# Kernel tuning notes

Hardware: AMD Instinct MI355X
Metric: run time of the kernel (lower is better)

## Reference

```python
import jax, jax.numpy as jnp
import numpy as np

B, N, P, E = 64, 512, 256, 4096          # batch, nodes (stations), partition nodes, edges
NUM_NWP, LP, F = 8, 16, 32               # num_nwp, local_points, local_cnn_dims
NT, ED, H, W = 8, 8, 64, 8               # num_temp, edge_feature_dims, decf_mlp_hidden, weight_function_dim
G, RH = 64, 256                          # gnn_dim, readout_hid_dim
H1, Q = 128, 9                           # mlp_hid_dim1, num quantiles


def setup_inputs() -> dict:
    key = jax.random.key(0)
    ks = iter(jax.random.split(key, 40))
    def rn(shape, s=0.05):
        return jax.random.normal(next(ks), shape, dtype=jnp.float32) * s
    # one-hot incidence matrices: each edge has one left (partition) node and one right node
    lidx = jax.random.randint(next(ks), (E,), 0, P)
    ridx = jax.random.randint(next(ks), (E,), 0, N)
    linc = jnp.zeros((P, E), jnp.float32).at[lidx, jnp.arange(E)].set(1.0)
    rinc = jnp.zeros((E, N), jnp.float32).at[jnp.arange(E), ridx].set(1.0)
    inp = {
        "x1": jax.random.normal(next(ks), (B, NUM_NWP * N, LP), dtype=jnp.float32),
        "x2": jax.random.normal(next(ks), (B, NT), dtype=jnp.float32),
        # LocalConv1D grouped conv (torch OIW layout: [Cout, Cin/groups, K])
        "conv_w": rn((F * N, NUM_NWP, LP)), "conv_b": rn((F * N,)),
        # WDSGCN2 edge-weight MLP
        "k1_w": rn((H, ED)), "k1_b": rn((H,)),
        "k2_w": rn((H, NT)),
        "k3_w": rn((H, F)),
        "k4_w": rn((H, F)),
        "k5_w": rn((W, H)), "k5_b": rn((W,)),
        "gc_w": rn((G, F * W)), "gc_b": rn((G,)),
        # readout
        "r0_w": rn((RH, G * P)),
        "r1_w": rn((RH, NT)), "r1_b": rn((RH,)),
        "r2_w": rn((RH, P)),
        "r3_w": rn((P, RH)), "r3_b": rn((P,)),
        # SMlp (forward uses l1 -> ELU -> l3 only)
        "l1_w": rn((H1, NT + G)), "l1_b": rn((H1,)),
        "l3_w": rn((Q, H1)), "l3_b": rn((Q,)),
        # buffers
        "ef": jax.random.normal(next(ks), (E, ED + 1), dtype=jnp.float32),
        "linc": linc,
        "rinc": rinc,
        "cap_feature": jax.random.normal(next(ks), (P,), dtype=jnp.float32),
        "partition_idx": jnp.arange(P, dtype=jnp.int32) * (N // P),
    }
    return inp


def reference(x1, x2, conv_w, conv_b, k1_w, k1_b, k2_w, k3_w, k4_w, k5_w, k5_b,
              gc_w, gc_b, r0_w, r1_w, r1_b, r2_w, r3_w, r3_b,
              l1_w, l1_b, l3_w, l3_b, ef, linc, rinc, cap_feature, partition_idx):
    b = x1.shape[0]
    # --- LocalConv1D: grouped conv1d (valid padding, output length 1) + ReLU ---
    y = jax.lax.conv_general_dilated(x1, conv_w, (1,), 'VALID',
                                     dimension_numbers=('NCH', 'OIH', 'NCH'),
                                     feature_group_count=N)
    x = jax.nn.relu(y + conv_b[None, :, None]).reshape(b, N, F)      # [B,N,F]
    # --- WDSGCN2: per-edge weight kernel ---
    kern = ef[:, :-1] @ k1_w.T + k1_b                                # [E,H]
    kern = kern[None] + (x2 @ k2_w.T)[:, None, :]                    # [B,E,H]
    xp = x[:, partition_idx, :]                                      # [B,P,F]
    kern = kern + jnp.einsum('pe,bpf->bef', linc, xp) @ k3_w.T       # left-node feats
    rx = jnp.einsum('en,bnf->bef', rinc, x)                          # right-node feats [B,E,F]
    kern = kern + rx @ k4_w.T
    kern = jax.nn.relu(jax.nn.leaky_relu(kern, 0.02) @ k5_w.T + k5_b)  # [B,E,W]
    # --- message = kernel (outer) right-node features, aggregated by left incidence ---
    msg = kern[:, :, :, None] * rx[:, :, None, :]                    # [B,E,W,F]
    agg = jnp.einsum('pe,bewf->bpwf', linc, msg).reshape(b, P, W * F)
    yg = jax.nn.relu(agg @ gc_w.T + gc_b)                            # [B,P,G]
    # --- readout attention over partition nodes ---
    h = yg.reshape(b, -1) @ r0_w.T + (x2 @ r1_w.T + r1_b) + cap_feature @ r2_w.T
    wt = jax.nn.relu(jax.nn.leaky_relu(h, 0.01) @ r3_w.T + r3_b)     # [B,P]
    res = jnp.einsum('bp,bpg->bg', wt, yg)                           # [B,G]
    # --- SMlp head ---
    z = jnp.concatenate([res, x2], axis=1)
    z = jax.nn.elu(z @ l1_w.T + l1_b)
    return z @ l3_w.T + l3_b                                         # [B,Q]
```

## Files before the change

kernel.cpp:

```cpp
#include <hip/hip_runtime.h>
#include <math.h>

#define B_ 64
#define N_ 512
#define P_ 256
#define E_ 4096
#define F_ 32
#define H_ 64
#define W_ 8
#define G_ 64
#define RH_ 256

#define X_OFF   0
#define T4_OFF  (X_OFF + N_*B_*F_)
#define T3_OFF  (T4_OFF + N_*B_*H_)
#define KB_OFF  (T3_OFF + P_*B_*H_)
#define KW_OFF  (KB_OFF + E_*H_)
#define YG_OFF  (KW_OFF + E_*B_*W_)
#define HB_OFF  (YG_OFF + B_*P_*G_)
#define RES_OFF (HB_OFF + B_*RH_)
#define INT_OFF (RES_OFF + 4*B_*G_)
#define PART_OFF (INT_OFF + 20480)

__global__ __launch_bounds__(256) void k_dc(const float* __restrict__ linc,
    const float* __restrict__ rinc, int* __restrict__ lidx, int* __restrict__ ridx,
    const float* __restrict__ x1, const float* __restrict__ conv_w,
    const float* __restrict__ conv_b, float* __restrict__ x) {
  __shared__ float wsm[32 * 132];
  __shared__ float xsm[8192];
  int blk = blockIdx.x, t = threadIdx.x;
  if (blk < 3072) {
    int i4 = blk * 256 + t;
    const int L4 = (P_ * E_) / 4;
    if (i4 < L4) {
      float4 v = ((const float4*)linc)[i4];
      int i = i4 * 4;
      int p = i >> 12, e = i & 4095;
      if (v.x != 0.0f) lidx[e]     = p;
      if (v.y != 0.0f) lidx[e + 1] = p;
      if (v.z != 0.0f) lidx[e + 2] = p;
      if (v.w != 0.0f) lidx[e + 3] = p;
    } else {
      int j4 = i4 - L4;
      float4 v = ((const float4*)rinc)[j4];
      int j = j4 * 4;
      int e = j >> 9, n = j & 511;
      if (v.x != 0.0f) ridx[e] = n;
      if (v.y != 0.0f) ridx[e] = n + 1;
      if (v.z != 0.0f) ridx[e] = n + 2;
      if (v.w != 0.0f) ridx[e] = n + 3;
    }
    return;
  }
  int n = blk - 3072;
  for (int i = t; i < 1024; i += 256) {
    int f = i >> 5, j = i & 31;
    ((float4*)wsm)[f * 33 + j] = ((const float4*)(conv_w + n * 4096))[i];
  }
  for (int i = t; i < 2048; i += 256) {
    int b = i >> 5, j = i & 31;
    ((float4*)xsm)[i] = ((const float4*)(x1 + b * 65536 + n * 128))[j];
  }
  __syncthreads();
  int f = t & 31, bq = t >> 5;
  float cb = conv_b[n * 32 + f];
  float acc[8];
#pragma unroll
  for (int bi = 0; bi < 8; bi++) acc[bi] = cb;
  const float4* wf4 = (const float4*)wsm + f * 33;
  const float4* xb4 = (const float4*)xsm + bq * 256;
#pragma unroll 4
  for (int k4 = 0; k4 < 32; k4++) {
    float4 wv = wf4[k4];
#pragma unroll
    for (int bi = 0; bi < 8; bi++) {
      float4 xv = xb4[bi * 32 + k4];
      acc[bi] += wv.x * xv.x + wv.y * xv.y + wv.z * xv.z + wv.w * xv.w;
    }
  }
#pragma unroll
  for (int bi = 0; bi < 8; bi++) {
    int b = bq * 8 + bi;
    x[n * 2048 + b * 32 + f] = fmaxf(acc[bi], 0.0f);
  }
}

__global__ __launch_bounds__(1024) void k_lists(const int* __restrict__ lidx,
    const int* __restrict__ ridx, int* __restrict__ part_start,
    int* __restrict__ part_edges, int* __restrict__ r_s) {
  __shared__ int cnt[256];
  __shared__ int buf[256];
  __shared__ int cur[256];
  int t = threadIdx.x;
  if (t < 256) cnt[t] = 0;
  __syncthreads();
  for (int e = t; e < E_; e += 1024) atomicAdd(&cnt[lidx[e]], 1);
  __syncthreads();
  if (t < 256) buf[t] = cnt[t];
  __syncthreads();
  for (int off = 1; off < 256; off <<= 1) {
    int add = 0;
    if (t < 256 && t >= off) add = buf[t - off];
    __syncthreads();
    if (t < 256) buf[t] += add;
    __syncthreads();
  }
  if (t < 256) {
    part_start[t + 1] = buf[t];
    if (t == 0) part_start[0] = 0;
    cur[t] = buf[t] - cnt[t];
  }
  __syncthreads();
  for (int e = t; e < E_; e += 1024) {
    int p = lidx[e];
    int pos = atomicAdd(&cur[p], 1);
    part_edges[pos] = e;
  }
  __syncthreads();
  for (int pos = t; pos < E_; pos += 1024) r_s[pos] = ridx[part_edges[pos]];
}

__global__ __launch_bounds__(256) void k_prep(
    const float* __restrict__ x, const int* __restrict__ pidx,
    const float* __restrict__ k3_w, const float* __restrict__ k4_w,
    const float* __restrict__ x2, const float* __restrict__ k2_w,
    const float* __restrict__ ef, const float* __restrict__ k1_w,
    const float* __restrict__ k1_b,
    const float* __restrict__ r1_w, const float* __restrict__ r1_b,
    const float* __restrict__ r2_w, const float* __restrict__ cap,
    float* __restrict__ t4, float* __restrict__ t3, float* __restrict__ kb,
    float* __restrict__ hbuf) {
  __shared__ float xsh[2048];
  __shared__ float wsh[64 * 36];
  __shared__ float x2s[512];
  __shared__ float k2s[512];
  int blk = blockIdx.x, t = threadIdx.x;
  if (blk < 768) {
    bool isT4 = blk < 512;
    int n = isT4 ? blk : pidx[blk - 512];
    const float* wmat = isT4 ? k4_w : k3_w;
    float* outp = isT4 ? (t4 + blk * 4096) : (t3 + (blk - 512) * 4096);
    for (int i = t; i < 512; i += 256) {
      ((float4*)xsh)[i] = ((const float4*)(x + n * 2048))[i];
      int h = i >> 3, j = i & 7;
      ((float4*)wsh)[h * 9 + j] = ((const float4*)wmat)[i];
    }
    if (isT4) {
      for (int i = t; i < 128; i += 256) {
        ((float4*)x2s)[i] = ((const float4*)x2)[i];
        ((float4*)k2s)[i] = ((const float4*)k2_w)[i];
      }
    }
    __syncthreads();
    int h = t & 63, bq = t >> 6;
    float wreg[32];
#pragma unroll
    for (int j = 0; j < 8; j++) {
      float4 v = ((float4*)wsh)[h * 9 + j];
      wreg[4 * j] = v.x; wreg[4 * j + 1] = v.y; wreg[4 * j + 2] = v.z; wreg[4 * j + 3] = v.w;
    }
    float w2[8];
    if (isT4) {
      float4 u = ((float4*)k2s)[h * 2], v = ((float4*)k2s)[h * 2 + 1];
      w2[0] = u.x; w2[1] = u.y; w2[2] = u.z; w2[3] = u.w;
      w2[4] = v.x; w2[5] = v.y; w2[6] = v.z; w2[7] = v.w;
    }
    for (int bi = 0; bi < 16; bi++) {
      int b = bq * 16 + bi;
      float acc = 0.0f;
#pragma unroll
      for (int j = 0; j < 8; j++) {
        float4 xv = ((float4*)xsh)[b * 8 + j];
        acc += xv.x * wreg[4 * j] + xv.y * wreg[4 * j + 1] +
               xv.z * wreg[4 * j + 2] + xv.w * wreg[4 * j + 3];
      }
      if (isT4) {
        float4 u = ((float4*)x2s)[b * 2], v = ((float4*)x2s)[b * 2 + 1];
        acc += u.x * w2[0] + u.y * w2[1] + u.z * w2[2] + u.w * w2[3] +
               v.x * w2[4] + v.y * w2[5] + v.z * w2[6] + v.w * w2[7];
      }
      outp[b * 64 + h] = acc;
    }
  } else if (blk < 1792) {
    int o = (blk - 768) * 256 + t;
    int e = o >> 6, h = o & 63;
    float acc = k1_b[h];
    const float* er = ef + e * 9;
    const float* kr = k1_w + h * 8;
#pragma unroll
    for (int d = 0; d < 8; d++) acc += er[d] * kr[d];
    kb[o] = acc;
  } else {
    int o = (blk - 1792) * 256 + t;
    int rh = o & 255;
    float acc = r1_b[rh];
    const float* xr = x2 + (o >> 8) * 8;
    const float* rr = r1_w + rh * 8;
#pragma unroll
    for (int d = 0; d < 8; d++) acc += xr[d] * rr[d];
    const float* r2r = r2_w + rh * 256;
    for (int p4 = 0; p4 < 64; p4++) {
      float4 cv = ((const float4*)cap)[p4];
      float4 rv = ((const float4*)r2r)[p4];
      acc += cv.x * rv.x + cv.y * rv.y + cv.z * rv.z + cv.w * rv.w;
    }
    hbuf[o] = acc;
  }
}

__global__ __launch_bounds__(256) void k_edge(
    const float* __restrict__ kb, const float* __restrict__ t3,
    const float* __restrict__ t4, const float* __restrict__ k5_w,
    const float* __restrict__ k5_b, const int* __restrict__ lidx,
    const int* __restrict__ ridx, const int* __restrict__ part_edges,
    float* __restrict__ kw_s) {
  __shared__ float k5t[4 * 520];
  int pos0 = blockIdx.x * 4, t = threadIdx.x;
  for (int i = t; i < 512; i += 256) {
    int h = i >> 3, w = i & 7;
    float v = k5_w[w * 64 + h];
#pragma unroll
    for (int qq = 0; qq < 4; qq++) k5t[qq * 520 + i] = v;
  }
  int q = t & 3, b = t >> 2;
  const float* kq = k5t + q * 520 + q * 128;
  float kb5_0 = k5_b[2 * q], kb5_1 = k5_b[2 * q + 1];
  __syncthreads();
  for (int ei = 0; ei < 4; ei++) {
    int pos = pos0 + ei;
    int e = part_edges[pos];
    int p = lidx[e], r = ridx[e];
    const float4* kb4 = (const float4*)(kb + e * 64 + q * 16);
    const float4* t34 = (const float4*)(t3 + p * 4096 + b * 64 + q * 16);
    const float4* t44 = (const float4*)(t4 + r * 4096 + b * 64 + q * 16);
    float lk[16];
#pragma unroll
    for (int j4 = 0; j4 < 4; j4++) {
      float4 a = kb4[j4], c = t34[j4], d = t44[j4];
      float v;
      v = a.x + c.x + d.x; lk[j4 * 4 + 0] = v > 0.0f ? v : 0.02f * v;
      v = a.y + c.y + d.y; lk[j4 * 4 + 1] = v > 0.0f ? v : 0.02f * v;
      v = a.z + c.z + d.z; lk[j4 * 4 + 2] = v > 0.0f ? v : 0.02f * v;
      v = a.w + c.w + d.w; lk[j4 * 4 + 3] = v > 0.0f ? v : 0.02f * v;
    }
    float pw[8] = {0, 0, 0, 0, 0, 0, 0, 0};
#pragma unroll
    for (int j = 0; j < 16; j++) {
      float4 u = *(const float4*)(kq + j * 8);
      float4 v = *(const float4*)(kq + j * 8 + 4);
      float l = lk[j];
      pw[0] += l * u.x; pw[1] += l * u.y; pw[2] += l * u.z; pw[3] += l * u.w;
      pw[4] += l * v.x; pw[5] += l * v.y; pw[6] += l * v.z; pw[7] += l * v.w;
    }
#pragma unroll
    for (int w = 0; w < 8; w++) {
      pw[w] += __shfl_xor(pw[w], 1);
      pw[w] += __shfl_xor(pw[w], 2);
    }
    float2 o;
    o.x = fmaxf(pw[2 * q] + kb5_0, 0.0f);
    o.y = fmaxf(pw[2 * q + 1] + kb5_1, 0.0f);
    *(float2*)(kw_s + pos * 512 + t * 2) = o;
  }
}

__global__ __launch_bounds__(256) void k_agg(
    const float* __restrict__ x, const float* __restrict__ kw_s,
    const int* __restrict__ r_s, const int* __restrict__ part_start,
    const float* __restrict__ gc_w, const float* __restrict__ gc_b,
    float* __restrict__ yg) {
  __shared__ float accS[32 * 256];
  int blk = blockIdx.x, t = threadIdx.x;
  int p = blk & 255, bsub = blk >> 8;
  int bl = t >> 3, s = t & 7;
  int b = bsub * 32 + bl;
  float acc[32];
#pragma unroll
  for (int j = 0; j < 32; j++) acc[j] = 0.0f;
  int s0 = part_start[p], s1 = part_start[p + 1];
  int r = (s0 < s1) ? r_s[s0] : 0;
  for (int pos = s0; pos < s1; pos++) {
    int r_n = (pos + 1 < s1) ? r_s[pos + 1] : 0;
    float kv = kw_s[pos * 512 + b * 8 + s];
    const float4* xp = (const float4*)(x + r * 2048 + b * 32);
    float4 x0 = xp[0], x1 = xp[1], x2 = xp[2], x3 = xp[3];
    float4 x4 = xp[4], x5 = xp[5], x6 = xp[6], x7 = xp[7];
    float xa[32];
    xa[0] = x0.x; xa[1] = x0.y; xa[2] = x0.z; xa[3] = x0.w;
    xa[4] = x1.x; xa[5] = x1.y; xa[6] = x1.z; xa[7] = x1.w;
    xa[8] = x2.x; xa[9] = x2.y; xa[10] = x2.z; xa[11] = x2.w;
    xa[12] = x3.x; xa[13] = x3.y; xa[14] = x3.z; xa[15] = x3.w;
    xa[16] = x4.x; xa[17] = x4.y; xa[18] = x4.z; xa[19] = x4.w;
    xa[20] = x5.x; xa[21] = x5.y; xa[22] = x5.z; xa[23] = x5.w;
    xa[24] = x6.x; xa[25] = x6.y; xa[26] = x6.z; xa[27] = x6.w;
    xa[28] = x7.x; xa[29] = x7.y; xa[30] = x7.z; xa[31] = x7.w;
#pragma unroll
    for (int j = 0; j < 32; j++) acc[j] += kv * xa[j];
    r = r_n;
  }
  int swz = bl >> 2;
#pragma unroll
  for (int j = 0; j < 4; j++) {
    int oct = s * 4 + j;
    int os = oct ^ swz;
    float* dst = accS + bl * 256 + os * 8;
    *(float4*)dst = make_float4(acc[j * 8], acc[j * 8 + 1], acc[j * 8 + 2], acc[j * 8 + 3]);
    *(float4*)(dst + 4) = make_float4(acc[j * 8 + 4], acc[j * 8 + 5], acc[j * 8 + 6], acc[j * 8 + 7]);
  }
  __syncthreads();
  int lane = t & 63, wv = t >> 6;
  int bg = lane >> 3, gg = lane & 7;
  int g0 = wv * 16 + gg * 2;
  const float* gw0 = gc_w + g0 * 256;
  const float* gw1 = gw0 + 256;
  float ac[4][2];
#pragma unroll
  for (int i = 0; i < 4; i++) { ac[i][0] = 0.0f; ac[i][1] = 0.0f; }
  for (int oct = 0; oct < 32; oct++) {
    float av[4][8];
#pragma unroll
    for (int i = 0; i < 4; i++) {
      int bli = bg * 4 + i;
      int os = oct ^ bg;
      const float* srcp = accS + bli * 256 + os * 8;
      float4 va = *(const float4*)srcp;
      float4 vb = *(const float4*)(srcp + 4);
      av[i][0] = va.x; av[i][1] = va.y; av[i][2] = va.z; av[i][3] = va.w;
      av[i][4] = vb.x; av[i][5] = vb.y; av[i][6] = vb.z; av[i][7] = vb.w;
    }
    float4 b0a = *(const float4*)(gw0 + oct * 8);
    float4 b0b = *(const float4*)(gw0 + oct * 8 + 4);
    float4 b1a = *(const float4*)(gw1 + oct * 8);
    float4 b1b = *(const float4*)(gw1 + oct * 8 + 4);
    float bv0[8] = {b0a.x, b0a.y, b0a.z, b0a.w, b0b.x, b0b.y, b0b.z, b0b.w};
    float bv1[8] = {b1a.x, b1a.y, b1a.z, b1a.w, b1b.x, b1b.y, b1b.z, b1b.w};
#pragma unroll
    for (int kk = 0; kk < 8; kk++) {
#pragma unroll
      for (int i = 0; i < 4; i++) {
        float a = av[i][kk];
        ac[i][0] += a * bv0[kk];
        ac[i][1] += a * bv1[kk];
      }
    }
  }
  float gb0 = gc_b[g0], gb1 = gc_b[g0 + 1];
#pragma unroll
  for (int i = 0; i < 4; i++) {
    int bb = bsub * 32 + bg * 4 + i;
    float2 o;
    o.x = fmaxf(ac[i][0] + gb0, 0.0f);
    o.y = fmaxf(ac[i][1] + gb1, 0.0f);
    *(float2*)(yg + bb * 16384 + p * 64 + g0) = o;
  }
}

__global__ __launch_bounds__(256) void k_r0(const float* __restrict__ yg,
    const float* __restrict__ r0_w, float* __restrict__ part) {
  __shared__ float ygs[32 * 69];
  __shared__ float wts[32 * 260];
  int kc = blockIdx.x, t = threadIdx.x;
  int k0 = kc * 32;
  {
    int c = t >> 5, rr = t & 31;
    for (int rd = 0; rd < 8; rd++) {
      int rh = rd * 32 + rr;
      float4 v = *(const float4*)(r0_w + rh * 16384 + k0 + c * 4);
      wts[(4 * c + 0) * 260 + rh] = v.x;
      wts[(4 * c + 1) * 260 + rh] = v.y;
      wts[(4 * c + 2) * 260 + rh] = v.z;
      wts[(4 * c + 3) * 260 + rh] = v.w;
    }
  }
  {
    int b = t >> 2, kq = t & 3;
    const float* src = yg + b * 16384 + k0 + kq * 8;
#pragma unroll
    for (int uu = 0; uu < 2; uu++) {
      float4 v = *(const float4*)(src + uu * 4);
      int kk = kq * 8 + uu * 4;
      ygs[(kk + 0) * 69 + b] = v.x;
      ygs[(kk + 1) * 69 + b] = v.y;
      ygs[(kk + 2) * 69 + b] = v.z;
      ygs[(kk + 3) * 69 + b] = v.w;
    }
  }
  __syncthreads();
  int lane = t & 63, wv = t >> 6;
  int b8 = lane & 7, r8 = lane >> 3;
  const float* yp = ygs + b8 * 8;
  const float* wp = wts + wv * 64 + r8 * 8;
  float acc[8][8];
#pragma unroll
  for (int i = 0; i < 8; i++)
#pragma unroll
    for (int j = 0; j < 8; j++) acc[i][j] = 0.0f;
#pragma unroll 2
  for (int k = 0; k < 32; k++) {
    float4 ya = *(const float4*)(yp + k * 69);
    float4 yb = *(const float4*)(yp + k * 69 + 4);
    float4 wa = *(const float4*)(wp + k * 260);
    float4 wb = *(const float4*)(wp + k * 260 + 4);
    float yv[8] = {ya.x, ya.y, ya.z, ya.w, yb.x, yb.y, yb.z, yb.w};
    float wr[8] = {wa.x, wa.y, wa.z, wa.w, wb.x, wb.y, wb.z, wb.w};
#pragma unroll
    for (int i = 0; i < 8; i++)
#pragma unroll
      for (int j = 0; j < 8; j++) acc[i][j] += yv[i] * wr[j];
  }
  float* pb = part + kc * 16384 + wv * 64 + r8 * 8;
#pragma unroll
  for (int i = 0; i < 8; i++) {
    float4 s0 = make_float4(acc[i][0], acc[i][1], acc[i][2], acc[i][3]);
    float4 s1 = make_float4(acc[i][4], acc[i][5], acc[i][6], acc[i][7]);
    float* pp = pb + (b8 * 8 + i) * 256;
    *(float4*)pp = s0;
    *(float4*)(pp + 4) = s1;
  }
}

__global__ __launch_bounds__(256) void k_r0red(const float* __restrict__ part,
    float* __restrict__ hbuf) {
  int blk = blockIdx.x;
  int oq = blk & 63, kq = blk >> 6;
  int o = oq * 256 + threadIdx.x;
  float s = 0.0f;
  const float* pp = part + kq * 64 * 16384 + o;
#pragma unroll 8
  for (int kc = 0; kc < 64; kc++) s += pp[kc * 16384];
  atomicAdd(&hbuf[o], s);
}

__global__ __launch_bounds__(256) void k_wt_res(const float* __restrict__ hbuf,
    const float* __restrict__ r3_w, const float* __restrict__ r3_b,
    const float* __restrict__ yg, float* __restrict__ res4) {
  __shared__ float hs[256];
  __shared__ float wts[64];
  __shared__ float red[256];
  int blk = blockIdx.x;
  int bb = blk >> 2, pq = blk & 3;
  int t = threadIdx.x;
  float hv = hbuf[bb * 256 + t];
  hs[t] = hv > 0.0f ? hv : 0.01f * hv;
  __syncthreads();
  int pl = t >> 2, c = t & 3;
  int pp = pq * 64 + pl;
  const float4* wrow = (const float4*)(r3_w + pp * 256 + c * 64);
  const float4* h4 = (const float4*)(hs) + c * 16;
  float a = 0.0f;
#pragma unroll
  for (int j = 0; j < 16; j++) {
    float4 w4 = wrow[j], hh = h4[j];
    a += hh.x * w4.x + hh.y * w4.y + hh.z * w4.z + hh.w * w4.w;
  }
  a += __shfl_xor(a, 1);
  a += __shfl_xor(a, 2);
  if (c == 0) wts[pl] = fmaxf(a + r3_b[pp], 0.0f);
  __syncthreads();
  int g = t & 63, ch = t >> 6;
  float r = 0.0f;
  const float* ygp = yg + bb * 16384 + pq * 4096 + g;
#pragma unroll
  for (int pi = 0; pi < 16; pi++) {
    int pl2 = ch * 16 + pi;
    r += wts[pl2] * ygp[pl2 * 64];
  }
  red[t] = r;
  __syncthreads();
  if (t < 64)
    res4[pq * 4096 + bb * 64 + t] = red[t] + red[t + 64] + red[t + 128] + red[t + 192];
}

__global__ __launch_bounds__(128) void k_final(const float* __restrict__ res4,
    const float* __restrict__ x2, const float* __restrict__ l1_w,
    const float* __restrict__ l1_b, const float* __restrict__ l3_w,
    const float* __restrict__ l3_b, float* __restrict__ out) {
  __shared__ float zs[128];
  int bb = blockIdx.x, t = threadIdx.x;
  float acc = l1_b[t];
  const float* wrow = l1_w + t * 72;
  const float* rr = res4 + bb * 64;
#pragma unroll 8
  for (int j = 0; j < 64; j++) {
    float rv = rr[j] + rr[4096 + j] + rr[8192 + j] + rr[12288 + j];
    acc += rv * wrow[j];
  }
  const float* xr = x2 + bb * 8;
#pragma unroll
  for (int j = 0; j < 8; j++) acc += xr[j] * wrow[64 + j];
  zs[t] = acc > 0.0f ? acc : expm1f(acc);
  __syncthreads();
  if (t < 9) {
    float o = l3_b[t];
    const float* w3 = l3_w + t * 128;
    for (int j = 0; j < 128; j++) o += zs[j] * w3[j];
    out[bb * 9 + t] = o;
  }
}

extern "C" void kernel_launch(void* const* d_in, const int* in_sizes, int n_in,
                              void* d_out, int out_size, void* d_ws, size_t ws_size,
                              hipStream_t stream) {
  (void)in_sizes; (void)n_in; (void)out_size; (void)ws_size;
  const float* x1     = (const float*)d_in[0];
  const float* x2     = (const float*)d_in[1];
  const float* conv_w = (const float*)d_in[2];
  const float* conv_b = (const float*)d_in[3];
  const float* k1_w   = (const float*)d_in[4];
  const float* k1_b   = (const float*)d_in[5];
  const float* k2_w   = (const float*)d_in[6];
  const float* k3_w   = (const float*)d_in[7];
  const float* k4_w   = (const float*)d_in[8];
  const float* k5_w   = (const float*)d_in[9];
  const float* k5_b   = (const float*)d_in[10];
  const float* gc_w   = (const float*)d_in[11];
  const float* gc_b   = (const float*)d_in[12];
  const float* r0_w   = (const float*)d_in[13];
  const float* r1_w   = (const float*)d_in[14];
  const float* r1_b   = (const float*)d_in[15];
  const float* r2_w   = (const float*)d_in[16];
  const float* r3_w   = (const float*)d_in[17];
  const float* r3_b   = (const float*)d_in[18];
  const float* l1_w   = (const float*)d_in[19];
  const float* l1_b   = (const float*)d_in[20];
  const float* l3_w   = (const float*)d_in[21];
  const float* l3_b   = (const float*)d_in[22];
  const float* ef     = (const float*)d_in[23];
  const float* linc   = (const float*)d_in[24];
  const float* rinc   = (const float*)d_in[25];
  const float* cap    = (const float*)d_in[26];
  const int*   pidx   = (const int*)d_in[27];
  float* out = (float*)d_out;

  float* ws   = (float*)d_ws;
  float* xbuf = ws + X_OFF;
  float* t4   = ws + T4_OFF;
  float* t3   = ws + T3_OFF;
  float* kb   = ws + KB_OFF;
  float* kw_s = ws + KW_OFF;
  float* yg   = ws + YG_OFF;
  float* hbuf = ws + HB_OFF;
  float* res4 = ws + RES_OFF;
  float* part = ws + PART_OFF;
  int* ib = (int*)(ws + INT_OFF);
  int* lidx = ib;
  int* ridx = ib + 4096;
  int* part_start = ib + 8192;
  int* part_edges = ib + 8704;
  int* r_s = ib + 12800;

  hipLaunchKernelGGL(k_dc, dim3(3584), dim3(256), 0, stream,
                     linc, rinc, lidx, ridx, x1, conv_w, conv_b, xbuf);
  hipLaunchKernelGGL(k_lists, dim3(1), dim3(1024), 0, stream,
                     lidx, ridx, part_start, part_edges, r_s);
  hipLaunchKernelGGL(k_prep, dim3(1856), dim3(256), 0, stream,
                     xbuf, pidx, k3_w, k4_w, x2, k2_w, ef, k1_w, k1_b,
                     r1_w, r1_b, r2_w, cap, t4, t3, kb, hbuf);
  hipLaunchKernelGGL(k_edge, dim3(1024), dim3(256), 0, stream,
                     kb, t3, t4, k5_w, k5_b, lidx, ridx, part_edges, kw_s);
  hipLaunchKernelGGL(k_agg, dim3(512), dim3(256), 0, stream,
                     xbuf, kw_s, r_s, part_start, gc_w, gc_b, yg);
  hipLaunchKernelGGL(k_r0, dim3(512), dim3(256), 0, stream, yg, r0_w, part);
  hipLaunchKernelGGL(k_r0red, dim3(512), dim3(256), 0, stream, part, hbuf);
  hipLaunchKernelGGL(k_wt_res, dim3(256), dim3(256), 0, stream, hbuf, r3_w, r3_b, yg, res4);
  hipLaunchKernelGGL(k_final, dim3(64), dim3(128), 0, stream,
                     res4, x2, l1_w, l1_b, l3_w, l3_b, out);
}
```

Measured before the change: 286.5 us.

## Split k_agg work across more blocks and unroll edge loop by four

The aggregation kernel now handles 16 batch rows per block instead of 32, with each thread covering half the feature dimension. This doubles the grid to 1024 blocks and halves the per-thread accumulator registers. The edge loop is unrolled by four so index and weight loads are batched ahead of the gathers, giving more memory-level parallelism. The cost is that gc_w is re-read by twice as many blocks, and each thread issues more separate gather loads.

```diff
diff --git a/kernel.cpp b/kernel.cpp
--- a/kernel.cpp
+++ b/kernel.cpp
@@ -269,90 +269,91 @@
     const int* __restrict__ r_s, const int* __restrict__ part_start,
     const float* __restrict__ gc_w, const float* __restrict__ gc_b,
     float* __restrict__ yg) {
-  __shared__ float accS[32 * 256];
+  __shared__ float accS[16 * 256];
   int blk = blockIdx.x, t = threadIdx.x;
   int p = blk & 255, bsub = blk >> 8;
-  int bl = t >> 3, s = t & 7;
-  int b = bsub * 32 + bl;
-  float acc[32];
-#pragma unroll
-  for (int j = 0; j < 32; j++) acc[j] = 0.0f;
+  int bl = t >> 4, s = t & 15;
+  int b = bsub * 16 + bl;
+  int w = s >> 1, fh = s & 1;
+  float acc[16];
+#pragma unroll
+  for (int j = 0; j < 16; j++) acc[j] = 0.0f;
   int s0 = part_start[p], s1 = part_start[p + 1];
-  int r = (s0 < s1) ? r_s[s0] : 0;
-  for (int pos = s0; pos < s1; pos++) {
-    int r_n = (pos + 1 < s1) ? r_s[pos + 1] : 0;
-    float kv = kw_s[pos * 512 + b * 8 + s];
-    const float4* xp = (const float4*)(x + r * 2048 + b * 32);
+  const float* xb = x + b * 32 + fh * 16;
+  const float* kwp = kw_s + b * 8 + w;
+  int pos = s0;
+  for (; pos + 3 < s1; pos += 4) {
+    int rr[4];
+    float kvv[4];
+    rr[0] = r_s[pos];     rr[1] = r_s[pos + 1];
+    rr[2] = r_s[pos + 2]; rr[3] = r_s[pos + 3];
+    kvv[0] = kwp[(pos) * 512];     kvv[1] = kwp[(pos + 1) * 512];
+    kvv[2] = kwp[(pos + 2) * 512]; kvv[3] = kwp[(pos + 3) * 512];
+#pragma unroll
+    for (int i = 0; i < 4; i++) {
+      const float4* xp = (const float4*)(xb + rr[i] * 2048);
+      float4 x0 = xp[0], x1 = xp[1], x2 = xp[2], x3 = xp[3];
+      float kv = kvv[i];
+      acc[0]  += kv * x0.x; acc[1]  += kv * x0.y; acc[2]  += kv * x0.z; acc[3]  += kv * x0.w;
+      acc[4]  += kv * x1.x; acc[5]  += kv * x1.y; acc[6]  += kv * x1.z; acc[7]  += kv * x1.w;
+      acc[8]  += kv * x2.x; acc[9]  += kv * x2.y; acc[10] += kv * x2.z; acc[11] += kv * x2.w;
+      acc[12] += kv * x3.x; acc[13] += kv * x3.y; acc[14] += kv * x3.z; acc[15] += kv * x3.w;
+    }
+  }
+  for (; pos < s1; pos++) {
+    int r = r_s[pos];
+    float kv = kwp[pos * 512];
+    const float4* xp = (const float4*)(xb + r * 2048);
     float4 x0 = xp[0], x1 = xp[1], x2 = xp[2], x3 = xp[3];
-    float4 x4 = xp[4], x5 = xp[5], x6 = xp[6], x7 = xp[7];
-    float xa[32];
-    xa[0] = x0.x; xa[1] = x0.y; xa[2] = x0.z; xa[3] = x0.w;
-    xa[4] = x1.x; xa[5] = x1.y; xa[6] = x1.z; xa[7] = x1.w;
-    xa[8] = x2.x; xa[9] = x2.y; xa[10] = x2.z; xa[11] = x2.w;
-    xa[12] = x3.x; xa[13] = x3.y; xa[14] = x3.z; xa[15] = x3.w;
-    xa[16] = x4.x; xa[17] = x4.y; xa[18] = x4.z; xa[19] = x4.w;
-    xa[20] = x5.x; xa[21] = x5.y; xa[22] = x5.z; xa[23] = x5.w;
-    xa[24] = x6.x; xa[25] = x6.y; xa[26] = x6.z; xa[27] = x6.w;
-    xa[28] = x7.x; xa[29] = x7.y; xa[30] = x7.z; xa[31] = x7.w;
-#pragma unroll
-    for (int j = 0; j < 32; j++) acc[j] += kv * xa[j];
-    r = r_n;
-  }
-  int swz = bl >> 2;
-#pragma unroll
-  for (int j = 0; j < 4; j++) {
-    int oct = s * 4 + j;
+    acc[0]  += kv * x0.x; acc[1]  += kv * x0.y; acc[2]  += kv * x0.z; acc[3]  += kv * x0.w;
+    acc[4]  += kv * x1.x; acc[5]  += kv * x1.y; acc[6]  += kv * x1.z; acc[7]  += kv * x1.w;
+    acc[8]  += kv * x2.x; acc[9]  += kv * x2.y; acc[10] += kv * x2.z; acc[11] += kv * x2.w;
+    acc[12] += kv * x3.x; acc[13] += kv * x3.y; acc[14] += kv * x3.z; acc[15] += kv * x3.w;
+  }
+  int swz = (bl >> 1) & 3;
+#pragma unroll
+  for (int j = 0; j < 2; j++) {
+    int oct = s * 2 + j;
     int os = oct ^ swz;
     float* dst = accS + bl * 256 + os * 8;
     *(float4*)dst = make_float4(acc[j * 8], acc[j * 8 + 1], acc[j * 8 + 2], acc[j * 8 + 3]);
-    *(float4*)(dst + 4) = make_float4(acc[j * 8 + 4], acc[j * 8 + 5], acc[j * 8 + 6], acc[j * 8 + 7]);
+    *(float4*)(dst + 4) =
+        make_float4(acc[j * 8 + 4], acc[j * 8 + 5], acc[j * 8 + 6], acc[j * 8 + 7]);
   }
   __syncthreads();
   int lane = t & 63, wv = t >> 6;
-  int bg = lane >> 3, gg = lane & 7;
+  int q = lane >> 3, gg = lane & 7;
   int g0 = wv * 16 + gg * 2;
   const float* gw0 = gc_w + g0 * 256;
   const float* gw1 = gw0 + 256;
-  float ac[4][2];
-#pragma unroll
-  for (int i = 0; i < 4; i++) { ac[i][0] = 0.0f; ac[i][1] = 0.0f; }
+  float ac00 = 0.0f, ac01 = 0.0f, ac10 = 0.0f, ac11 = 0.0f;
+  int row0 = q * 2, row1 = q * 2 + 1;
+  int sz = q & 3;
   for (int oct = 0; oct < 32; oct++) {
-    float av[4][8];
-#pragma unroll
-    for (int i = 0; i < 4; i++) {
-      int bli = bg * 4 + i;
-      int os = oct ^ bg;
-      const float* srcp = accS + bli * 256 + os * 8;
-      float4 va = *(const float4*)srcp;
-      float4 vb = *(const float4*)(srcp + 4);
-      av[i][0] = va.x; av[i][1] = va.y; av[i][2] = va.z; av[i][3] = va.w;
-      av[i][4] = vb.x; av[i][5] = vb.y; av[i][6] = vb.z; av[i][7] = vb.w;
-    }
-    float4 b0a = *(const float4*)(gw0 + oct * 8);
-    float4 b0b = *(const float4*)(gw0 + oct * 8 + 4);
-    float4 b1a = *(const float4*)(gw1 + oct * 8);
-    float4 b1b = *(const float4*)(gw1 + oct * 8 + 4);
+    int os = oct ^ sz;
+    const float* s0p = accS + row0 * 256 + os * 8;
+    const float* s1p = accS + row1 * 256 + os * 8;
+    float4 a0a = *(const float4*)s0p, a0b = *(const float4*)(s0p + 4);
+    float4 a1a = *(const float4*)s1p, a1b = *(const float4*)(s1p + 4);
+    float4 b0a = *(const float4*)(gw0 + oct * 8), b0b = *(const float4*)(gw0 + oct * 8 + 4);
+    float4 b1a = *(const float4*)(gw1 + oct * 8), b1b = *(const float4*)(gw1 + oct * 8 + 4);
+    float av0[8] = {a0a.x, a0a.y, a0a.z, a0a.w, a0b.x, a0b.y, a0b.z, a0b.w};
+    float av1[8] = {a1a.x, a1a.y, a1a.z, a1a.w, a1b.x, a1b.y, a1b.z, a1b.w};
     float bv0[8] = {b0a.x, b0a.y, b0a.z, b0a.w, b0b.x, b0b.y, b0b.z, b0b.w};
     float bv1[8] = {b1a.x, b1a.y, b1a.z, b1a.w, b1b.x, b1b.y, b1b.z, b1b.w};
 #pragma unroll
     for (int kk = 0; kk < 8; kk++) {
-#pragma unroll
-      for (int i = 0; i < 4; i++) {
-        float a = av[i][kk];
-        ac[i][0] += a * bv0[kk];
-        ac[i][1] += a * bv1[kk];
-      }
+      ac00 += av0[kk] * bv0[kk]; ac01 += av0[kk] * bv1[kk];
+      ac10 += av1[kk] * bv0[kk]; ac11 += av1[kk] * bv1[kk];
     }
   }
   float gb0 = gc_b[g0], gb1 = gc_b[g0 + 1];
-#pragma unroll
-  for (int i = 0; i < 4; i++) {
-    int bb = bsub * 32 + bg * 4 + i;
-    float2 o;
-    o.x = fmaxf(ac[i][0] + gb0, 0.0f);
-    o.y = fmaxf(ac[i][1] + gb1, 0.0f);
-    *(float2*)(yg + bb * 16384 + p * 64 + g0) = o;
-  }
+  int b0 = bsub * 16 + row0, b1 = bsub * 16 + row1;
+  float2 o0, o1;
+  o0.x = fmaxf(ac00 + gb0, 0.0f); o0.y = fmaxf(ac01 + gb1, 0.0f);
+  o1.x = fmaxf(ac10 + gb0, 0.0f); o1.y = fmaxf(ac11 + gb1, 0.0f);
+  *(float2*)(yg + b0 * 16384 + p * 64 + g0) = o0;
+  *(float2*)(yg + b1 * 16384 + p * 64 + g0) = o1;
 }
 
 __global__ __launch_bounds__(256) void k_r0(const float* __restrict__ yg,
@@ -558,7 +559,7 @@
                      r1_w, r1_b, r2_w, cap, t4, t3, kb, hbuf);
   hipLaunchKernelGGL(k_edge, dim3(1024), dim3(256), 0, stream,
                      kb, t3, t4, k5_w, k5_b, lidx, ridx, part_edges, kw_s);
-  hipLaunchKernelGGL(k_agg, dim3(512), dim3(256), 0, stream,
+  hipLaunchKernelGGL(k_agg, dim3(1024), dim3(256), 0, stream,
                      xbuf, kw_s, r_s, part_start, gc_w, gc_b, yg);
   hipLaunchKernelGGL(k_r0, dim3(512), dim3(256), 0, stream, yg, r0_w, part);
   hipLaunchKernelGGL(k_r0red, dim3(512), dim3(256), 0, stream, part, hbuf);
```

Measured after the change: 305.5 us. 1.07x slower.
